# Kernel tuning notes

Measured on AMD Instinct MI355X. Metric: run time of the kernel, lower is better.

## Reference

```python
import jax, jax.numpy as jnp
import numpy as np

N_NODES = 50000
N_EDGES = 800000
IN_CH = 128
HEADS = 4
HEAD_DIM = 32  # out_channels // heads = 128 // 4
OUT_CH = HEADS * HEAD_DIM
NEG_SLOPE = 0.2
LN_EPS = 1e-5


def setup_inputs() -> dict:
    key = jax.random.key(0)
    ks = jax.random.split(key, 10)
    s = 1.0 / np.sqrt(IN_CH)
    return {
        "x": jax.random.normal(ks[0], (N_NODES, IN_CH), jnp.float32),
        "edge_index": jax.random.randint(ks[1], (2, N_EDGES), 0, N_NODES, dtype=jnp.int64),
        "W_l": jax.random.normal(ks[2], (IN_CH, OUT_CH), jnp.float32) * s,
        "b_l": jnp.zeros((OUT_CH,), jnp.float32),
        "W_r": jax.random.normal(ks[3], (IN_CH, OUT_CH), jnp.float32) * s,
        "b_r": jnp.zeros((OUT_CH,), jnp.float32),
        "att": jax.random.normal(ks[4], (HEADS, HEAD_DIM), jnp.float32) * (1.0 / np.sqrt(HEAD_DIM)),
        "bias": jnp.zeros((OUT_CH,), jnp.float32),
        "gamma": jnp.ones((OUT_CH,), jnp.float32),
        "beta": jnp.zeros((OUT_CH,), jnp.float32),
    }


def reference(x, edge_index, W_l, b_l, W_r, b_r, att, bias, gamma, beta):
    N = x.shape[0]
    H, C = att.shape
    # add self loops (PyG GATv2Conv default add_self_loops=True)
    loops = jnp.arange(N, dtype=edge_index.dtype)
    src = jnp.concatenate([edge_index[0], loops])  # source j
    dst = jnp.concatenate([edge_index[1], loops])  # target i
    # separate source/target transforms (share_weights=False)
    xl = (x @ W_l + b_l).reshape(N, H, C)  # source features
    xr = (x @ W_r + b_r).reshape(N, H, C)  # target features
    # GATv2 attention: e_ij = att . leaky_relu(xl_j + xr_i)
    e = xl[src] + xr[dst]                              # [E', H, C]
    e = jnp.where(e > 0, e, NEG_SLOPE * e)             # leaky_relu(0.2)
    score = jnp.einsum('ehc,hc->eh', e, att)           # [E', H]
    # segment softmax over edges sharing the same destination node
    smax = jax.ops.segment_max(score, dst, num_segments=N)      # [N, H]
    score = jnp.exp(score - smax[dst])
    denom = jax.ops.segment_sum(score, dst, num_segments=N)     # [N, H]
    alpha = score / denom[dst]                                   # [E', H]
    # weighted scatter-sum of source messages
    msg = alpha[:, :, None] * xl[src]                            # [E', H, C]
    out = jax.ops.segment_sum(msg, dst, num_segments=N)          # [N, H, C]
    out = out.reshape(N, H * C) + bias
    # SiLU
    out = out * jax.nn.sigmoid(out)
    # LayerNorm over feature dim
    mu = jnp.mean(out, axis=-1, keepdims=True)
    var = jnp.mean(jnp.square(out - mu), axis=-1, keepdims=True)
    out = (out - mu) * jax.lax.rsqrt(var + LN_EPS) * gamma + beta
    return out
```

## Files before the change

### kernel.cpp

```cpp
#include <hip/hip_runtime.h>
#include <hip/hip_fp16.h>
#include <math.h>

#define CH 128
#define NEG_SLOPE 0.2f
#define LN_EPS 1e-5f
#define CAP 64

typedef _Float16 f16;
typedef _Float16 f16x2 __attribute__((ext_vector_type(2)));
typedef _Float16 f16x4 __attribute__((ext_vector_type(4)));
typedef _Float16 f16x8 __attribute__((ext_vector_type(8)));
typedef float    f32x4 __attribute__((ext_vector_type(4)));
typedef int      i32x4 __attribute__((ext_vector_type(4)));

__global__ void k_init(const float* __restrict__ Wl, const float* __restrict__ Wr,
                       f16* __restrict__ Wt, int* __restrict__ cnt, int N)
{
    int tid = blockIdx.x * 256 + threadIdx.x;
    if (tid < 256 * CH) {
        int k   = tid >> 8;
        int col = tid & 255;
        float w = (col < CH) ? Wl[k * CH + col] : Wr[k * CH + (col - CH)];
        Wt[(size_t)col * CH + k] = (f16)w;
    }
    if (tid < N) cnt[tid] = 0;
}

__global__ __launch_bounds__(256) void k_transform(
    const float* __restrict__ x, const f16* __restrict__ Wt,
    const float* __restrict__ bl, const float* __restrict__ br,
    f16* __restrict__ xlh, f16* __restrict__ xrh, int N)
{
    const int wave = (blockIdx.x * 256 + threadIdx.x) >> 6;
    const int lane = threadIdx.x & 63;
    const int m0   = wave * 16;
    if (m0 >= N) return;

    const int n16  = lane & 15;
    const int quad = lane >> 4;

    f16x8 xfr[4];
    {
        int mrow = m0 + n16; if (mrow >= N) mrow = N - 1;
        const float* xrow = x + (size_t)mrow * CH + quad * 8;
#pragma unroll
        for (int ks = 0; ks < 4; ++ks) {
            float4 p0 = *(const float4*)(xrow + ks * 32);
            float4 p1 = *(const float4*)(xrow + ks * 32 + 4);
            f16x8 f; f[0] = (f16)p0.x; f[1] = (f16)p0.y; f[2] = (f16)p0.z; f[3] = (f16)p0.w;
                     f[4] = (f16)p1.x; f[5] = (f16)p1.y; f[6] = (f16)p1.z; f[7] = (f16)p1.w;
            xfr[ks] = f;
        }
    }

#pragma unroll
    for (int ct = 0; ct < 16; ++ct) {
        f32x4 acc = {0.f, 0.f, 0.f, 0.f};
        const int acol = ct * 16 + n16;
        const f16* wp = Wt + (size_t)acol * CH + quad * 8;
#pragma unroll
        for (int ks = 0; ks < 4; ++ks) {
            f16x8 afr = *(const f16x8*)(wp + ks * 32);
            acc = __builtin_amdgcn_mfma_f32_16x16x32_f16(afr, xfr[ks], acc, 0, 0, 0);
        }
        const int node = m0 + n16;
        const int chq  = ct * 16 + quad * 4;
        if (node < N) {
            if (ct < 8) {
                float4 bv = *(const float4*)&bl[chq];
                f16x4 pk = {(f16)(acc[0] + bv.x), (f16)(acc[1] + bv.y),
                            (f16)(acc[2] + bv.z), (f16)(acc[3] + bv.w)};
                *(f16x4*)(xlh + (size_t)node * CH + chq) = pk;
            } else {
                int cc = chq - CH;
                float4 bv = *(const float4*)&br[cc];
                f16x4 pk = {(f16)(acc[0] + bv.x), (f16)(acc[1] + bv.y),
                            (f16)(acc[2] + bv.z), (f16)(acc[3] + bv.w)};
                *(f16x4*)(xrh + (size_t)node * CH + cc) = pk;
            }
        }
    }
}

#define FILL_EPB 4096
__global__ __launch_bounds__(256) void k_fill(
    const int* __restrict__ ei, int E, unsigned CM,
    int* __restrict__ cnt, int* __restrict__ col)
{
    const int cls = blockIdx.x & 7;
    const int sl  = blockIdx.x >> 3;
    const int base = sl * FILL_EPB + threadIdx.x * 4;

#pragma unroll
    for (int i = 0; i < 4; ++i) {
        int e = base + i * 1024;
        if (e < E) {
            i32x4 dv = __builtin_nontemporal_load((const i32x4*)&ei[E + e]);
            i32x4 sv = __builtin_nontemporal_load((const i32x4*)&ei[e]);
#pragma unroll
            for (int k = 0; k < 4; ++k) {
                int d = dv[k];
                if ((int)__umulhi((unsigned)d, CM) == cls) {
                    int pos = atomicAdd(&cnt[d], 1);
                    if (pos < CAP) col[((size_t)d << 6) + pos] = sv[k];
                }
            }
        }
    }
}

__global__ __launch_bounds__(256) void k_aggregate(
    const f16* __restrict__ xlh, const f16* __restrict__ xrh,
    const int* __restrict__ col, const int* __restrict__ cnt,
    const float* __restrict__ att, const float* __restrict__ bias,
    const float* __restrict__ gamma, const float* __restrict__ beta,
    float* __restrict__ out, int N)
{
    const int lane = threadIdx.x & 63;
    const int wid  = threadIdx.x >> 6;
    const int nsub = lane >> 5;
    const int g    = (lane >> 4) & 1;
    const int l16  = lane & 15;
    const int c0   = l16 * 8;

    const int nraw = blockIdx.x * 8 + wid * 2 + nsub;
    if (blockIdx.x * 8 >= N) return;
    const int n  = (nraw < N) ? nraw : N - 1;
    const int n6 = n << 6;

    int cn = cnt[n]; cn = cn < CAP ? cn : CAP;
    const int cnA = __builtin_amdgcn_readlane(cn, 0);
    const int cnB = __builtin_amdgcn_readlane(cn, 32);
    const int cmax = cnA > cnB ? cnA : cnB;

    f16x8 xr8, at8;
    {
        xr8 = *(const f16x8*)(xrh + (size_t)n * CH + c0);
        float4 a0 = *(const float4*)&att[c0];
        float4 a1 = *(const float4*)&att[c0 + 4];
        const float L2E = 1.44269504f;
        at8[0]=(f16)(a0.x*L2E); at8[1]=(f16)(a0.y*L2E);
        at8[2]=(f16)(a0.z*L2E); at8[3]=(f16)(a0.w*L2E);
        at8[4]=(f16)(a1.x*L2E); at8[5]=(f16)(a1.y*L2E);
        at8[6]=(f16)(a1.z*L2E); at8[7]=(f16)(a1.w*L2E);
    }
    const f16x8 c02 = {(f16)NEG_SLOPE,(f16)NEG_SLOPE,(f16)NEG_SLOPE,(f16)NEG_SLOPE,
                       (f16)NEG_SLOPE,(f16)NEG_SLOPE,(f16)NEG_SLOPE,(f16)NEG_SLOPE};

    float l_run = 0.f;
    float acc[8] = {0.f,0.f,0.f,0.f,0.f,0.f,0.f,0.f};

    {
        f16x8 u = *(const f16x8*)(xlh + ((size_t)n << 7) + c0);
        f16x8 tt = u + xr8;
        f16x8 lk = __builtin_elementwise_max(tt, tt * c02);
        union { f16x8 v; f16x2 h[4]; } L, A;
        L.v = lk; A.v = at8;
        float s = __builtin_amdgcn_fdot2(L.h[0], A.h[0], 0.f, false);
        s = __builtin_amdgcn_fdot2(L.h[1], A.h[1], s, false);
        s = __builtin_amdgcn_fdot2(L.h[2], A.h[2], s, false);
        s = __builtin_amdgcn_fdot2(L.h[3], A.h[3], s, false);
        int t;
        t = __builtin_amdgcn_update_dpp(0, __builtin_bit_cast(int, s), 0xB1, 0xF, 0xF, false);
        s += __builtin_bit_cast(float, t);
        t = __builtin_amdgcn_update_dpp(0, __builtin_bit_cast(int, s), 0x4E, 0xF, 0xF, false);
        s += __builtin_bit_cast(float, t);
        float w;
        asm("v_exp_f32 %0, %1" : "=v"(w) : "v"(s));
        w = (g == 0) ? w : 0.f;
        l_run = w;
#pragma unroll
        for (int j = 0; j < 8; ++j) acc[j] = (float)u[j] * w;
    }

    int idx[4];
#pragma unroll
    for (int i = 0; i < 4; ++i) idx[i] = col[n6 + 2 * i + g];

    for (int t0 = 0; t0 < cmax; t0 += 8) {
        f16x8 u[4];
#pragma unroll
        for (int i = 0; i < 4; ++i) {
            unsigned su = (unsigned)idx[i];
            su = (su < (unsigned)N) ? su : 0u;
            u[i] = *(const f16x8*)(xlh + ((size_t)su << 7) + c0);
        }
#pragma unroll
        for (int i = 0; i < 4; ++i) idx[i] = col[n6 + t0 + 8 + 2 * i + g];
#pragma unroll
        for (int i = 0; i < 4; ++i) {
            f16x8 tt = u[i] + xr8;
            f16x8 lk = __builtin_elementwise_max(tt, tt * c02);
            union { f16x8 v; f16x2 h[4]; } L, A;
            L.v = lk; A.v = at8;
            float s = __builtin_amdgcn_fdot2(L.h[0], A.h[0], 0.f, false);
            s = __builtin_amdgcn_fdot2(L.h[1], A.h[1], s, false);
            s = __builtin_amdgcn_fdot2(L.h[2], A.h[2], s, false);
            s = __builtin_amdgcn_fdot2(L.h[3], A.h[3], s, false);
            int t;
            t = __builtin_amdgcn_update_dpp(0, __builtin_bit_cast(int, s), 0xB1, 0xF, 0xF, false);
            s += __builtin_bit_cast(float, t);
            t = __builtin_amdgcn_update_dpp(0, __builtin_bit_cast(int, s), 0x4E, 0xF, 0xF, false);
            s += __builtin_bit_cast(float, t);
            float w;
            asm("v_exp_f32 %0, %1" : "=v"(w) : "v"(s));
            w = (t0 + 2 * i + g < cn) ? w : 0.f;
            l_run += w;
#pragma unroll
            for (int j = 0; j < 8; ++j) acc[j] += (float)u[i][j] * w;
        }
    }

    l_run += __shfl_xor(l_run, 16);
#pragma unroll
    for (int j = 0; j < 8; ++j) acc[j] += __shfl_xor(acc[j], 16);

    if (g == 0 && nraw < N) {
        const float inv = 1.f / l_run;
        float4 b0 = *(const float4*)&bias[c0];
        float4 b1 = *(const float4*)&bias[c0 + 4];
        float y[8];
        y[0] = acc[0]*inv + b0.x; y[1] = acc[1]*inv + b0.y;
        y[2] = acc[2]*inv + b0.z; y[3] = acc[3]*inv + b0.w;
        y[4] = acc[4]*inv + b1.x; y[5] = acc[5]*inv + b1.y;
        y[6] = acc[6]*inv + b1.z; y[7] = acc[7]*inv + b1.w;
        float s1 = 0.f, s2 = 0.f;
#pragma unroll
        for (int j = 0; j < 8; ++j) {
            y[j] = y[j] / (1.f + __expf(-y[j]));
            s1 += y[j];
            s2 += y[j] * y[j];
        }
#pragma unroll
        for (int off = 1; off < 16; off <<= 1) {
            s1 += __shfl_xor(s1, off);
            s2 += __shfl_xor(s2, off);
        }
        float mu   = s1 * (1.f / 128.f);
        float var  = s2 * (1.f / 128.f) - mu * mu;
        float rstd = rsqrtf(var + LN_EPS);
        float4 g0 = *(const float4*)&gamma[c0];
        float4 g1 = *(const float4*)&gamma[c0 + 4];
        float4 e0 = *(const float4*)&beta[c0];
        float4 e1 = *(const float4*)&beta[c0 + 4];
        float4 o0, o1;
        o0.x = (y[0]-mu)*rstd*g0.x + e0.x;  o0.y = (y[1]-mu)*rstd*g0.y + e0.y;
        o0.z = (y[2]-mu)*rstd*g0.z + e0.z;  o0.w = (y[3]-mu)*rstd*g0.w + e0.w;
        o1.x = (y[4]-mu)*rstd*g1.x + e1.x;  o1.y = (y[5]-mu)*rstd*g1.y + e1.y;
        o1.z = (y[6]-mu)*rstd*g1.z + e1.z;  o1.w = (y[7]-mu)*rstd*g1.w + e1.w;
        float* orow = out + (size_t)n * CH + c0;
        *(float4*)orow       = o0;
        *(float4*)(orow + 4) = o1;
    }
}

extern "C" void kernel_launch(void* const* d_in, const int* in_sizes, int n_in,
                              void* d_out, int out_size, void* d_ws, size_t ws_size,
                              hipStream_t stream)
{
    const float* x    = (const float*)d_in[0];
    const int*   ei   = (const int*)  d_in[1];
    const float* Wl   = (const float*)d_in[2];
    const float* bl   = (const float*)d_in[3];
    const float* Wr   = (const float*)d_in[4];
    const float* br   = (const float*)d_in[5];
    const float* att  = (const float*)d_in[6];
    const float* bias = (const float*)d_in[7];
    const float* gam  = (const float*)d_in[8];
    const float* bet  = (const float*)d_in[9];
    float* out = (float*)d_out;

    const int N = in_sizes[0] / CH;
    const int E = in_sizes[1] / 2;

    char* ws = (char*)d_ws;
    size_t off = 0;
    auto carve = [&](size_t bytes) -> char* {
        char* p = ws + off;
        off += (bytes + 255) & ~(size_t)255;
        return p;
    };
    f16* xlh  = (f16*)carve((size_t)N * CH * sizeof(f16));
    f16* xrh  = (f16*)carve((size_t)N * CH * sizeof(f16));
    f16* Wt   = (f16*)carve((size_t)256 * CH * sizeof(f16));
    int* cnt  = (int*)carve((size_t)N * sizeof(int));
    int* col  = (int*)carve(((size_t)N * CAP + 16) * sizeof(int));
    (void)ws_size;

    const int nwaves = (N + 15) / 16;
    const int TB     = (nwaves * 64 + 255) / 256;
    const int IB     = (((N > 256 * CH ? N : 256 * CH) + 255) / 256);

    const unsigned CM = (unsigned)(((8ULL << 32) + (unsigned)N - 1) / (unsigned)N);
    const int S  = (E + FILL_EPB - 1) / FILL_EPB;
    const int FB = 8 * S;

    k_init      <<<IB, 256, 0, stream>>>(Wl, Wr, Wt, cnt, N);
    k_transform <<<TB, 256, 0, stream>>>(x, Wt, bl, br, xlh, xrh, N);
    k_fill      <<<FB, 256, 0, stream>>>(ei, E, CM, cnt, col);
    k_aggregate <<<(N + 7) / 8, 256, 0, stream>>>(xlh, xrh, col, cnt,
                                                  att, bias, gam, bet, out, N);
}
```

Baseline: 209.6 us.

## Fuse weight transpose and count init into transform kernel via LDS staging

Removes the separate init kernel that transposed W_l/W_r into an fp16 global buffer and zeroed counts. Each transform block now loads W_l, then W_r, converts them to fp16 into a swizzled shared-memory tile, and runs the MFMA products from LDS. Count zeroing moves into the transform kernel too. This saves one launch and the global weight round trip, but every block now reloads and converts both weight matrices and adds several barriers.

```diff
diff --git a/kernel.cpp b/kernel.cpp
--- a/kernel.cpp
+++ b/kernel.cpp
@@ -14,34 +14,30 @@
 typedef float    f32x4 __attribute__((ext_vector_type(4)));
 typedef int      i32x4 __attribute__((ext_vector_type(4)));
 
-__global__ void k_init(const float* __restrict__ Wl, const float* __restrict__ Wr,
-                       f16* __restrict__ Wt, int* __restrict__ cnt, int N)
+__global__ __launch_bounds__(256) void k_transform(
+    const float* __restrict__ x,
+    const float* __restrict__ Wl, const float* __restrict__ Wr,
+    const float* __restrict__ bl, const float* __restrict__ br,
+    f16* __restrict__ xlh, f16* __restrict__ xrh,
+    int* __restrict__ cnt, int N)
 {
-    int tid = blockIdx.x * 256 + threadIdx.x;
-    if (tid < 256 * CH) {
-        int k   = tid >> 8;
-        int col = tid & 255;
-        float w = (col < CH) ? Wl[k * CH + col] : Wr[k * CH + (col - CH)];
-        Wt[(size_t)col * CH + k] = (f16)w;
-    }
-    if (tid < N) cnt[tid] = 0;
-}
-
-__global__ __launch_bounds__(256) void k_transform(
-    const float* __restrict__ x, const f16* __restrict__ Wt,
-    const float* __restrict__ bl, const float* __restrict__ br,
-    f16* __restrict__ xlh, f16* __restrict__ xrh, int N)
-{
+    __shared__ f16 WtL[128 * CH];
+
+    {
+        int idx = blockIdx.x * 256 + threadIdx.x;
+        if (idx < N) cnt[idx] = 0;
+    }
+
     const int wave = (blockIdx.x * 256 + threadIdx.x) >> 6;
     const int lane = threadIdx.x & 63;
     const int m0   = wave * 16;
-    if (m0 >= N) return;
+    const bool active = (m0 < N);
 
     const int n16  = lane & 15;
     const int quad = lane >> 4;
 
     f16x8 xfr[4];
-    {
+    if (active) {
         int mrow = m0 + n16; if (mrow >= N) mrow = N - 1;
         const float* xrow = x + (size_t)mrow * CH + quad * 8;
 #pragma unroll
@@ -54,30 +50,74 @@
         }
     }
 
-#pragma unroll
-    for (int ct = 0; ct < 16; ++ct) {
-        f32x4 acc = {0.f, 0.f, 0.f, 0.f};
-        const int acol = ct * 16 + n16;
-        const f16* wp = Wt + (size_t)acol * CH + quad * 8;
-#pragma unroll
-        for (int ks = 0; ks < 4; ++ks) {
-            f16x8 afr = *(const f16x8*)(wp + ks * 32);
-            acc = __builtin_amdgcn_mfma_f32_16x16x32_f16(afr, xfr[ks], acc, 0, 0, 0);
-        }
-        const int node = m0 + n16;
-        const int chq  = ct * 16 + quad * 4;
-        if (node < N) {
-            if (ct < 8) {
+    const int kbase = threadIdx.x >> 5;
+    const int col4  = (threadIdx.x & 31) * 4;
+
+#pragma unroll
+    for (int r = 0; r < 16; ++r) {
+        int k = kbase + (r << 3);
+        float4 v = *(const float4*)&Wl[k * CH + col4];
+#pragma unroll
+        for (int j = 0; j < 4; ++j) {
+            int c = col4 + j;
+            WtL[c * CH + (k ^ ((c & 7) << 3))] = (f16)((&v.x)[j]);
+        }
+    }
+    __syncthreads();
+
+    if (active) {
+#pragma unroll
+        for (int ct = 0; ct < 8; ++ct) {
+            f32x4 acc = {0.f, 0.f, 0.f, 0.f};
+            const int colA = ct * 16 + n16;
+#pragma unroll
+            for (int ks = 0; ks < 4; ++ks) {
+                f16x8 afr = *(const f16x8*)&WtL[colA * CH +
+                                ((quad * 8 + ks * 32) ^ ((colA & 7) << 3))];
+                acc = __builtin_amdgcn_mfma_f32_16x16x32_f16(afr, xfr[ks], acc, 0, 0, 0);
+            }
+            const int node = m0 + n16;
+            const int chq  = ct * 16 + quad * 4;
+            if (node < N) {
                 float4 bv = *(const float4*)&bl[chq];
                 f16x4 pk = {(f16)(acc[0] + bv.x), (f16)(acc[1] + bv.y),
                             (f16)(acc[2] + bv.z), (f16)(acc[3] + bv.w)};
                 *(f16x4*)(xlh + (size_t)node * CH + chq) = pk;
-            } else {
-                int cc = chq - CH;
-                float4 bv = *(const float4*)&br[cc];
+            }
+        }
+    }
+    __syncthreads();
+
+#pragma unroll
+    for (int r = 0; r < 16; ++r) {
+        int k = kbase + (r << 3);
+        float4 v = *(const float4*)&Wr[k * CH + col4];
+#pragma unroll
+        for (int j = 0; j < 4; ++j) {
+            int c = col4 + j;
+            WtL[c * CH + (k ^ ((c & 7) << 3))] = (f16)((&v.x)[j]);
+        }
+    }
+    __syncthreads();
+
+    if (active) {
+#pragma unroll
+        for (int ct = 0; ct < 8; ++ct) {
+            f32x4 acc = {0.f, 0.f, 0.f, 0.f};
+            const int colA = ct * 16 + n16;
+#pragma unroll
+            for (int ks = 0; ks < 4; ++ks) {
+                f16x8 afr = *(const f16x8*)&WtL[colA * CH +
+                                ((quad * 8 + ks * 32) ^ ((colA & 7) << 3))];
+                acc = __builtin_amdgcn_mfma_f32_16x16x32_f16(afr, xfr[ks], acc, 0, 0, 0);
+            }
+            const int node = m0 + n16;
+            const int chq  = ct * 16 + quad * 4;
+            if (node < N) {
+                float4 bv = *(const float4*)&br[chq];
                 f16x4 pk = {(f16)(acc[0] + bv.x), (f16)(acc[1] + bv.y),
                             (f16)(acc[2] + bv.z), (f16)(acc[3] + bv.w)};
-                *(f16x4*)(xrh + (size_t)node * CH + cc) = pk;
+                *(f16x4*)(xrh + (size_t)node * CH + chq) = pk;
             }
         }
     }
@@ -283,21 +323,18 @@
     };
     f16* xlh  = (f16*)carve((size_t)N * CH * sizeof(f16));
     f16* xrh  = (f16*)carve((size_t)N * CH * sizeof(f16));
-    f16* Wt   = (f16*)carve((size_t)256 * CH * sizeof(f16));
     int* cnt  = (int*)carve((size_t)N * sizeof(int));
     int* col  = (int*)carve(((size_t)N * CAP + 16) * sizeof(int));
     (void)ws_size;
 
     const int nwaves = (N + 15) / 16;
     const int TB     = (nwaves * 64 + 255) / 256;
-    const int IB     = (((N > 256 * CH ? N : 256 * CH) + 255) / 256);
 
     const unsigned CM = (unsigned)(((8ULL << 32) + (unsigned)N - 1) / (unsigned)N);
     const int S  = (E + FILL_EPB - 1) / FILL_EPB;
     const int FB = 8 * S;
 
-    k_init      <<<IB, 256, 0, stream>>>(Wl, Wr, Wt, cnt, N);
-    k_transform <<<TB, 256, 0, stream>>>(x, Wt, bl, br, xlh, xrh, N);
+    k_transform <<<TB, 256, 0, stream>>>(x, Wl, Wr, bl, br, xlh, xrh, cnt, N);
     k_fill      <<<FB, 256, 0, stream>>>(ei, E, CM, cnt, col);
     k_aggregate <<<(N + 7) / 8, 256, 0, stream>>>(xlh, xrh, col, cnt,
                                                   att, bias, gam, bet, out, N);
```

New measurement: 211.4 us. Within noise of the previous version (+0.9%).
